# Kernel optimization log

Measured on AMD Instinct MI355X. Metric: run time of the kernel, lower is better.

Reference implementation:

```python
import jax, jax.numpy as jnp
import numpy as np

# --- static configuration (mirrors init_kwargs) ---
L = 16        # latent_size
HL = 512      # hypernet_layer_size
D = 64        # decoder_layer_size
NDEC = 2      # decoder_n_layers
B, G = 128, 100  # batch, grid (pressure levels)
LOGP_MEAN, LOGP_STD = 0.0, 3.0
T_MEAN, T_STD = 1500.0, 500.0

# decoder layer structure generated by the hypernet
WEIGHT_SIZES = [(1, D)] + [(D, D)] * NDEC + [(D, 1)]
BIAS_SIZES = [1] + [D] * NDEC + [1]
OUT_SIZE = sum(a * b for a, b in WEIGHT_SIZES) + sum(BIAS_SIZES)  # 8450


def setup_inputs() -> dict:
    key = jax.random.key(0)
    ks = jax.random.split(key, 8)
    def init(k, shape, fan_in):
        return (jax.random.normal(k, shape, jnp.float32) / np.float32(np.sqrt(fan_in)))
    return {
        "z": jax.random.normal(ks[0], (B, L), jnp.float32),
        "log_P": jax.random.normal(ks[1], (B, G), jnp.float32) * 2.0,
        # hypernet MLP params: L -> HL -> HL -> HL -> OUT_SIZE
        "hW0": init(ks[2], (L, HL), L), "hb0": jnp.zeros((HL,), jnp.float32),
        "hW1": init(ks[3], (HL, HL), HL), "hb1": jnp.zeros((HL,), jnp.float32),
        "hW2": init(ks[4], (HL, HL), HL), "hb2": jnp.zeros((HL,), jnp.float32),
        "hWo": init(ks[5], (HL, OUT_SIZE), HL), "hbo": jnp.zeros((OUT_SIZE,), jnp.float32),
    }


def reference(z, log_P, hW0, hb0, hW1, hb1, hW2, hb2, hWo, hbo):
    Bsz, Gsz = log_P.shape
    R = Bsz * Gsz  # flattened rows
    # broadcast latent over the pressure grid: (B, L) -> (R, L)
    z_flat = jnp.broadcast_to(z[:, None, :], (Bsz, Gsz, z.shape[-1])).reshape(R, -1)
    # normalize pressure -> decoder input, shape (R, 1)
    x = (log_P.reshape(R, 1) - LOGP_MEAN) / LOGP_STD
    # hypernet MLP (leaky_relu, slope 0.01 like torch default)
    h = jax.nn.leaky_relu(z_flat @ hW0 + hb0)
    h = jax.nn.leaky_relu(h @ hW1 + hb1)
    h = jax.nn.leaky_relu(h @ hW2 + hb2)
    wab = h @ hWo + hbo  # (R, OUT_SIZE): per-row decoder weights+biases
    # per-row decoder: chain of batched GEMVs with siren activation
    off = 0
    n_layers = len(WEIGHT_SIZES)
    for i, ((di, do), bs) in enumerate(zip(WEIGHT_SIZES, BIAS_SIZES)):
        n = di * do
        w = wab[:, off:off + n].reshape(R, di, do)
        b = wab[:, off + n:off + n + bs]  # broadcasts against (R, do)
        off += n + bs
        x = jnp.einsum('bi,bij->bj', x, w) + b
        if i == 0:
            x = x * 30.0  # siren first-layer omega_0
        if i < n_layers - 1:
            x = jnp.sin(x)  # siren activation; last layer is Identity
    T_pred = x.reshape(Bsz, Gsz)
    # undo temperature normalization
    return T_pred * T_STD + T_MEAN
```

## Files before the change

kernel.cpp:

```cpp
#include <hip/hip_runtime.h>

#define WSTRIDE 8704
#define DSTR 68

__device__ __forceinline__ float lrelu(float x) { return x > 0.0f ? x : 0.01f * x; }

__global__ __launch_bounds__(128) void h0T_kernel(const float* __restrict__ z,
                                                  const float* __restrict__ W,
                                                  const float* __restrict__ bias,
                                                  float* __restrict__ h0T) {
    int j = blockIdx.x;
    int b = threadIdx.x;
    float zr[16];
    *(float4*)&zr[0]  = *(const float4*)&z[b * 16 + 0];
    *(float4*)&zr[4]  = *(const float4*)&z[b * 16 + 4];
    *(float4*)&zr[8]  = *(const float4*)&z[b * 16 + 8];
    *(float4*)&zr[12] = *(const float4*)&z[b * 16 + 12];
    float acc = bias[j];
#pragma unroll
    for (int l = 0; l < 16; ++l) acc = fmaf(zr[l], W[l * 512 + j], acc);
    h0T[j * 128 + b] = lrelu(acc);
}

__global__ __launch_bounds__(512) void gemmT_kernel(const float* __restrict__ At,
                                                    const float* __restrict__ W,
                                                    const float* __restrict__ bias,
                                                    float* __restrict__ OT) {
    __shared__ float red[8][64][13];
    int jt = blockIdx.x & 7;
    int bt = blockIdx.x >> 3;
    int lane = threadIdx.x & 63;
    int wid  = __builtin_amdgcn_readfirstlane(threadIdx.x >> 6);
    int j = jt * 64 + lane;
    int b0 = bt * 8;
    float acc[8] = {};
    int k0 = wid * 64;
#pragma unroll 4
    for (int kk = 0; kk < 64; ++kk) {
        int k = k0 + kk;
        const float* __restrict__ a = At + k * 128 + b0;
        float w = W[k * 512 + j];
#pragma unroll
        for (int i = 0; i < 8; ++i) acc[i] = fmaf(a[i], w, acc[i]);
    }
#pragma unroll
    for (int i = 0; i < 8; ++i) red[wid][lane][i] = acc[i];
    __syncthreads();
    int jj = threadIdx.x >> 3;
    int bb = threadIdx.x & 7;
    float s = 0.f;
#pragma unroll
    for (int w = 0; w < 8; ++w) s += red[w][jj][bb];
    int jg = jt * 64 + jj;
    OT[jg * 128 + b0 + bb] = lrelu(s + bias[jg]);
}

__global__ __launch_bounds__(256) void wabT_kernel(const float* __restrict__ At,
                                                   const float* __restrict__ W,
                                                   const float* __restrict__ bias,
                                                   float* __restrict__ wab) {
    __shared__ float red[4][128][13];
    int tid = threadIdx.x;
    if (blockIdx.x == 1152) {
        int b = tid & 127;
        int jc = 8448 + (tid >> 7);
        float acc = 0.f;
#pragma unroll 8
        for (int k = 0; k < 512; ++k)
            acc = fmaf(At[k * 128 + b], W[k * 8450 + jc], acc);
        wab[b * WSTRIDE + jc] = acc + bias[jc];
        return;
    }
    int xcd = blockIdx.x & 7;
    int idx = blockIdx.x >> 3;
    int jt = (idx >> 4) * 8 + xcd;
    int bt = idx & 15;
    if (jt >= 66) return;
    int lane = tid & 63;
    int wid  = __builtin_amdgcn_readfirstlane(tid >> 6);
    int j = jt * 128 + lane * 2;
    int b0 = bt * 8;
    float acc[8][2] = {};
    int k0 = wid * 128;
#pragma unroll 4
    for (int kk = 0; kk < 128; ++kk) {
        int k = k0 + kk;
        const float* __restrict__ a = At + k * 128 + b0;
        float2 w = *(const float2*)&W[k * 8450 + j];
#pragma unroll
        for (int i = 0; i < 8; ++i) {
            acc[i][0] = fmaf(a[i], w.x, acc[i][0]);
            acc[i][1] = fmaf(a[i], w.y, acc[i][1]);
        }
    }
#pragma unroll
    for (int i = 0; i < 8; ++i) {
        red[wid][lane * 2 + 0][i] = acc[i][0];
        red[wid][lane * 2 + 1][i] = acc[i][1];
    }
    __syncthreads();
    int jj = tid & 127;
    int half = tid >> 7;
    int jg = jt * 128 + jj;
    float bj = bias[jg];
#pragma unroll
    for (int q = 0; q < 4; ++q) {
        int bb = half * 4 + q;
        float s = red[0][jj][bb] + red[1][jj][bb] + red[2][jj][bb] + red[3][jj][bb];
        wab[(b0 + bb) * WSTRIDE + jg] = s + bj;
    }
}

__global__ __launch_bounds__(256) void decoder_kernel(const float* __restrict__ wab,
                                                      const float* __restrict__ logP,
                                                      float* __restrict__ out) {
    __shared__ __align__(16) float hA[64 * DSTR];
    __shared__ __align__(16) float hB[64 * DSTR];
    __shared__ float red[4][68];
    int b   = blockIdx.x >> 1;
    int gbl = blockIdx.x & 1;
    int lane = threadIdx.x & 63;
    int wid  = __builtin_amdgcn_readfirstlane(threadIdx.x >> 6);
    int jq = wid * 16;
    int g = gbl * 64 + lane;
    bool act = g < 100;
    const float* __restrict__ row = wab + b * WSTRIDE;
    float x0 = act ? logP[b * 100 + g] * (1.0f / 3.0f) : 0.0f;

    float c0 = row[64];
#pragma unroll
    for (int t4 = 0; t4 < 4; ++t4) {
        float4 v;
        v.x = __sinf(30.0f * fmaf(x0, row[jq + t4*4 + 0], c0));
        v.y = __sinf(30.0f * fmaf(x0, row[jq + t4*4 + 1], c0));
        v.z = __sinf(30.0f * fmaf(x0, row[jq + t4*4 + 2], c0));
        v.w = __sinf(30.0f * fmaf(x0, row[jq + t4*4 + 3], c0));
        *(float4*)&hA[lane * DSTR + jq + t4 * 4] = v;
    }
    __syncthreads();

    {
        float a[16];
#pragma unroll
        for (int t = 0; t < 16; ++t) a[t] = row[4161 + jq + t];
#pragma unroll 4
        for (int i4 = 0; i4 < 16; ++i4) {
            float4 hv = *(const float4*)&hA[lane * DSTR + i4 * 4];
#pragma unroll
            for (int e = 0; e < 4; ++e) {
                int i = i4 * 4 + e;
                const float* __restrict__ wr = row + 65 + i * 64 + jq;
                float hi = (&hv.x)[e];
#pragma unroll
                for (int t = 0; t < 16; ++t) a[t] = fmaf(hi, wr[t], a[t]);
            }
        }
#pragma unroll
        for (int t4 = 0; t4 < 4; ++t4) {
            float4 v;
            v.x = __sinf(a[t4*4 + 0]); v.y = __sinf(a[t4*4 + 1]);
            v.z = __sinf(a[t4*4 + 2]); v.w = __sinf(a[t4*4 + 3]);
            *(float4*)&hB[lane * DSTR + jq + t4 * 4] = v;
        }
    }
    __syncthreads();

    {
        float a[16];
#pragma unroll
        for (int t = 0; t < 16; ++t) a[t] = row[8321 + jq + t];
#pragma unroll 4
        for (int i4 = 0; i4 < 16; ++i4) {
            float4 hv = *(const float4*)&hB[lane * DSTR + i4 * 4];
#pragma unroll
            for (int e = 0; e < 4; ++e) {
                int i = i4 * 4 + e;
                const float* __restrict__ wr = row + 4225 + i * 64 + jq;
                float hi = (&hv.x)[e];
#pragma unroll
                for (int t = 0; t < 16; ++t) a[t] = fmaf(hi, wr[t], a[t]);
            }
        }
#pragma unroll
        for (int t4 = 0; t4 < 4; ++t4) {
            float4 v;
            v.x = __sinf(a[t4*4 + 0]); v.y = __sinf(a[t4*4 + 1]);
            v.z = __sinf(a[t4*4 + 2]); v.w = __sinf(a[t4*4 + 3]);
            *(float4*)&hA[lane * DSTR + jq + t4 * 4] = v;
        }
    }
    __syncthreads();

    float p = 0.f;
#pragma unroll
    for (int t4 = 0; t4 < 4; ++t4) {
        float4 hv = *(const float4*)&hA[lane * DSTR + jq + t4 * 4];
        p = fmaf(hv.x, row[8385 + jq + t4*4 + 0], p);
        p = fmaf(hv.y, row[8385 + jq + t4*4 + 1], p);
        p = fmaf(hv.z, row[8385 + jq + t4*4 + 2], p);
        p = fmaf(hv.w, row[8385 + jq + t4*4 + 3], p);
    }
    red[wid][lane] = p;
    __syncthreads();
    if (wid == 0 && act) {
        float s = red[0][lane] + red[1][lane] + red[2][lane] + red[3][lane] + row[8449];
        out[b * 100 + g] = fmaf(s, 500.0f, 1500.0f);
    }
}

extern "C" void kernel_launch(void* const* d_in, const int* in_sizes, int n_in,
                              void* d_out, int out_size, void* d_ws, size_t ws_size,
                              hipStream_t stream) {
    const float* z    = (const float*)d_in[0];
    const float* logP = (const float*)d_in[1];
    const float* hW0  = (const float*)d_in[2];
    const float* hb0  = (const float*)d_in[3];
    const float* hW1  = (const float*)d_in[4];
    const float* hb1  = (const float*)d_in[5];
    const float* hW2  = (const float*)d_in[6];
    const float* hb2  = (const float*)d_in[7];
    const float* hWo  = (const float*)d_in[8];
    const float* hbo  = (const float*)d_in[9];
    float* out = (float*)d_out;

    float* wab = (float*)d_ws;
    float* h0T = wab + 128 * WSTRIDE;
    float* h1T = h0T + 512 * 128;
    float* h2T = h1T + 512 * 128;

    h0T_kernel<<<512, 128, 0, stream>>>(z, hW0, hb0, h0T);
    gemmT_kernel<<<128, 512, 0, stream>>>(h0T, hW1, hb1, h1T);
    gemmT_kernel<<<128, 512, 0, stream>>>(h1T, hW2, hb2, h2T);
    wabT_kernel<<<1153, 256, 0, stream>>>(h2T, hWo, hbo, wab);
    decoder_kernel<<<256, 256, 0, stream>>>(wab, logP, out);
}
```

Before: 74.99 us.

## Stage activations and decoder weights in LDS, retile hypernet GEMMs

The hidden-layer GEMMs now stage the activation tile in shared memory and use 4 batch rows per block with 256 threads, doubling the grid. The output GEMM stages a 16-row activation tile in LDS, uses 16x2 register tiles per thread, and halves the block count with a new XCD-aware mapping. The decoder copies each 64x64 weight matrix into LDS once and reads it with vectorized broadcast loads instead of repeated global loads, and stores hidden states transposed with a padded stride. This adds LDS traffic and extra syncs, and the output GEMM has less parallelism.

```diff
diff --git a/kernel.cpp b/kernel.cpp
--- a/kernel.cpp
+++ b/kernel.cpp
@@ -1,7 +1,7 @@
 #include <hip/hip_runtime.h>
 
 #define WSTRIDE 8704
-#define DSTR 68
+#define GSTR 65
 
 __device__ __forceinline__ float lrelu(float x) { return x > 0.0f ? x : 0.01f * x; }
 
@@ -22,35 +22,44 @@
     h0T[j * 128 + b] = lrelu(acc);
 }
 
-__global__ __launch_bounds__(512) void gemmT_kernel(const float* __restrict__ At,
+__global__ __launch_bounds__(256) void gemmT_kernel(const float* __restrict__ At,
                                                     const float* __restrict__ W,
                                                     const float* __restrict__ bias,
                                                     float* __restrict__ OT) {
-    __shared__ float red[8][64][13];
+    __shared__ __align__(16) float As[512][4];
+    __shared__ float red[4][64][5];
     int jt = blockIdx.x & 7;
     int bt = blockIdx.x >> 3;
-    int lane = threadIdx.x & 63;
-    int wid  = __builtin_amdgcn_readfirstlane(threadIdx.x >> 6);
+    int tid = threadIdx.x;
+    int lane = tid & 63;
+    int wid  = __builtin_amdgcn_readfirstlane(tid >> 6);
+    int b0 = bt * 4;
+#pragma unroll
+    for (int r = 0; r < 4; ++r) {
+        int p = r * 256 + tid;
+        int k = p >> 1, q = p & 1;
+        *(float2*)&As[k][q * 2] = *(const float2*)&At[k * 128 + b0 + q * 2];
+    }
+    __syncthreads();
     int j = jt * 64 + lane;
-    int b0 = bt * 8;
-    float acc[8] = {};
-    int k0 = wid * 64;
-#pragma unroll 4
-    for (int kk = 0; kk < 64; ++kk) {
+    float acc[4] = {};
+    int k0 = wid * 128;
+#pragma unroll 8
+    for (int kk = 0; kk < 128; ++kk) {
         int k = k0 + kk;
-        const float* __restrict__ a = At + k * 128 + b0;
+        float4 a = *(const float4*)&As[k][0];
         float w = W[k * 512 + j];
-#pragma unroll
-        for (int i = 0; i < 8; ++i) acc[i] = fmaf(a[i], w, acc[i]);
-    }
-#pragma unroll
-    for (int i = 0; i < 8; ++i) red[wid][lane][i] = acc[i];
-    __syncthreads();
-    int jj = threadIdx.x >> 3;
-    int bb = threadIdx.x & 7;
-    float s = 0.f;
-#pragma unroll
-    for (int w = 0; w < 8; ++w) s += red[w][jj][bb];
+        acc[0] = fmaf(a.x, w, acc[0]);
+        acc[1] = fmaf(a.y, w, acc[1]);
+        acc[2] = fmaf(a.z, w, acc[2]);
+        acc[3] = fmaf(a.w, w, acc[3]);
+    }
+#pragma unroll
+    for (int i = 0; i < 4; ++i) red[wid][lane][i] = acc[i];
+    __syncthreads();
+    int jj = tid >> 2;
+    int bb = tid & 3;
+    float s = red[0][jj][bb] + red[1][jj][bb] + red[2][jj][bb] + red[3][jj][bb];
     int jg = jt * 64 + jj;
     OT[jg * 128 + b0 + bb] = lrelu(s + bias[jg]);
 }
@@ -59,54 +68,73 @@
                                                    const float* __restrict__ W,
                                                    const float* __restrict__ bias,
                                                    float* __restrict__ wab) {
-    __shared__ float red[4][128][13];
+    __shared__ __align__(16) float As[512][16];
+    __shared__ float red[4][64][33];
     int tid = threadIdx.x;
-    if (blockIdx.x == 1152) {
+    if (blockIdx.x == 528) {
         int b = tid & 127;
         int jc = 8448 + (tid >> 7);
-        float acc = 0.f;
-#pragma unroll 8
-        for (int k = 0; k < 512; ++k)
-            acc = fmaf(At[k * 128 + b], W[k * 8450 + jc], acc);
-        wab[b * WSTRIDE + jc] = acc + bias[jc];
+        float a0 = 0.f, a1 = 0.f, a2 = 0.f, a3 = 0.f;
+#pragma unroll 4
+        for (int k4 = 0; k4 < 128; ++k4) {
+            a0 = fmaf(At[(k4*4+0) * 128 + b], W[(k4*4+0) * 8450 + jc], a0);
+            a1 = fmaf(At[(k4*4+1) * 128 + b], W[(k4*4+1) * 8450 + jc], a1);
+            a2 = fmaf(At[(k4*4+2) * 128 + b], W[(k4*4+2) * 8450 + jc], a2);
+            a3 = fmaf(At[(k4*4+3) * 128 + b], W[(k4*4+3) * 8450 + jc], a3);
+        }
+        wab[b * WSTRIDE + jc] = a0 + a1 + a2 + a3 + bias[jc];
         return;
     }
-    int xcd = blockIdx.x & 7;
-    int idx = blockIdx.x >> 3;
-    int jt = (idx >> 4) * 8 + xcd;
-    int bt = idx & 15;
-    if (jt >= 66) return;
+    int v = (blockIdx.x & 7) * 66 + (blockIdx.x >> 3);
+    int jt = v >> 3;
+    int bt = v & 7;
     int lane = tid & 63;
     int wid  = __builtin_amdgcn_readfirstlane(tid >> 6);
-    int j = jt * 128 + lane * 2;
-    int b0 = bt * 8;
-    float acc[8][2] = {};
+    int b0 = bt * 16;
+#pragma unroll
+    for (int r = 0; r < 16; ++r) {
+        int p = r * 256 + tid;
+        int k = p >> 3, q = p & 7;
+        *(float2*)&As[k][q * 2] = *(const float2*)&At[k * 128 + b0 + q * 2];
+    }
+    __syncthreads();
+    int j0 = jt * 128 + lane * 2;
+    float acc[16][2] = {};
     int k0 = wid * 128;
 #pragma unroll 4
     for (int kk = 0; kk < 128; ++kk) {
         int k = k0 + kk;
-        const float* __restrict__ a = At + k * 128 + b0;
-        float2 w = *(const float2*)&W[k * 8450 + j];
-#pragma unroll
-        for (int i = 0; i < 8; ++i) {
-            acc[i][0] = fmaf(a[i], w.x, acc[i][0]);
-            acc[i][1] = fmaf(a[i], w.y, acc[i][1]);
-        }
-    }
-#pragma unroll
-    for (int i = 0; i < 8; ++i) {
-        red[wid][lane * 2 + 0][i] = acc[i][0];
-        red[wid][lane * 2 + 1][i] = acc[i][1];
-    }
-    __syncthreads();
-    int jj = tid & 127;
-    int half = tid >> 7;
+        float4 a0 = *(const float4*)&As[k][0];
+        float4 a1 = *(const float4*)&As[k][4];
+        float4 a2 = *(const float4*)&As[k][8];
+        float4 a3 = *(const float4*)&As[k][12];
+        float2 w = *(const float2*)&W[k * 8450 + j0];
+        float av[16] = {a0.x,a0.y,a0.z,a0.w, a1.x,a1.y,a1.z,a1.w,
+                        a2.x,a2.y,a2.z,a2.w, a3.x,a3.y,a3.z,a3.w};
+#pragma unroll
+        for (int bb = 0; bb < 16; ++bb) {
+            acc[bb][0] = fmaf(av[bb], w.x, acc[bb][0]);
+            acc[bb][1] = fmaf(av[bb], w.y, acc[bb][1]);
+        }
+    }
+#pragma unroll
+    for (int bb = 0; bb < 16; ++bb) {
+        red[wid][lane][bb * 2 + 0] = acc[bb][0];
+        red[wid][lane][bb * 2 + 1] = acc[bb][1];
+    }
+    __syncthreads();
+    int jj = tid >> 1;
+    int bh = tid & 1;
+    int lane_r = jj >> 1;
+    int jl = jj & 1;
     int jg = jt * 128 + jj;
     float bj = bias[jg];
 #pragma unroll
-    for (int q = 0; q < 4; ++q) {
-        int bb = half * 4 + q;
-        float s = red[0][jj][bb] + red[1][jj][bb] + red[2][jj][bb] + red[3][jj][bb];
+    for (int bq = 0; bq < 8; ++bq) {
+        int bb = bh * 8 + bq;
+        int idx = bb * 2 + jl;
+        float s = red[0][lane_r][idx] + red[1][lane_r][idx]
+                + red[2][lane_r][idx] + red[3][lane_r][idx];
         wab[(b0 + bb) * WSTRIDE + jg] = s + bj;
     }
 }
@@ -114,13 +142,15 @@
 __global__ __launch_bounds__(256) void decoder_kernel(const float* __restrict__ wab,
                                                       const float* __restrict__ logP,
                                                       float* __restrict__ out) {
-    __shared__ __align__(16) float hA[64 * DSTR];
-    __shared__ __align__(16) float hB[64 * DSTR];
+    __shared__ __align__(16) float Wl[64 * 64];
+    __shared__ float hX[64 * GSTR];
+    __shared__ float hY[64 * GSTR];
     __shared__ float red[4][68];
     int b   = blockIdx.x >> 1;
     int gbl = blockIdx.x & 1;
-    int lane = threadIdx.x & 63;
-    int wid  = __builtin_amdgcn_readfirstlane(threadIdx.x >> 6);
+    int tid = threadIdx.x;
+    int lane = tid & 63;
+    int wid  = __builtin_amdgcn_readfirstlane(tid >> 6);
     int jq = wid * 16;
     int g = gbl * 64 + lane;
     bool act = g < 100;
@@ -129,13 +159,12 @@
 
     float c0 = row[64];
 #pragma unroll
-    for (int t4 = 0; t4 < 4; ++t4) {
-        float4 v;
-        v.x = __sinf(30.0f * fmaf(x0, row[jq + t4*4 + 0], c0));
-        v.y = __sinf(30.0f * fmaf(x0, row[jq + t4*4 + 1], c0));
-        v.z = __sinf(30.0f * fmaf(x0, row[jq + t4*4 + 2], c0));
-        v.w = __sinf(30.0f * fmaf(x0, row[jq + t4*4 + 3], c0));
-        *(float4*)&hA[lane * DSTR + jq + t4 * 4] = v;
+    for (int t = 0; t < 16; ++t)
+        hX[(jq + t) * GSTR + lane] = __sinf(30.0f * fmaf(x0, row[jq + t], c0));
+#pragma unroll
+    for (int r = 0; r < 16; ++r) {
+        int idx = r * 256 + tid;
+        Wl[idx] = row[65 + idx];
     }
     __syncthreads();
 
@@ -144,24 +173,30 @@
 #pragma unroll
         for (int t = 0; t < 16; ++t) a[t] = row[4161 + jq + t];
 #pragma unroll 4
-        for (int i4 = 0; i4 < 16; ++i4) {
-            float4 hv = *(const float4*)&hA[lane * DSTR + i4 * 4];
-#pragma unroll
-            for (int e = 0; e < 4; ++e) {
-                int i = i4 * 4 + e;
-                const float* __restrict__ wr = row + 65 + i * 64 + jq;
-                float hi = (&hv.x)[e];
-#pragma unroll
-                for (int t = 0; t < 16; ++t) a[t] = fmaf(hi, wr[t], a[t]);
-            }
-        }
-#pragma unroll
-        for (int t4 = 0; t4 < 4; ++t4) {
-            float4 v;
-            v.x = __sinf(a[t4*4 + 0]); v.y = __sinf(a[t4*4 + 1]);
-            v.z = __sinf(a[t4*4 + 2]); v.w = __sinf(a[t4*4 + 3]);
-            *(float4*)&hB[lane * DSTR + jq + t4 * 4] = v;
-        }
+        for (int i = 0; i < 64; ++i) {
+            float hi = hX[i * GSTR + lane];
+            const float* wr = &Wl[i * 64 + jq];
+            float4 w0 = *(const float4*)&wr[0];
+            float4 w1 = *(const float4*)&wr[4];
+            float4 w2 = *(const float4*)&wr[8];
+            float4 w3 = *(const float4*)&wr[12];
+            a[0]  = fmaf(hi, w0.x, a[0]);  a[1]  = fmaf(hi, w0.y, a[1]);
+            a[2]  = fmaf(hi, w0.z, a[2]);  a[3]  = fmaf(hi, w0.w, a[3]);
+            a[4]  = fmaf(hi, w1.x, a[4]);  a[5]  = fmaf(hi, w1.y, a[5]);
+            a[6]  = fmaf(hi, w1.z, a[6]);  a[7]  = fmaf(hi, w1.w, a[7]);
+            a[8]  = fmaf(hi, w2.x, a[8]);  a[9]  = fmaf(hi, w2.y, a[9]);
+            a[10] = fmaf(hi, w2.z, a[10]); a[11] = fmaf(hi, w2.w, a[11]);
+            a[12] = fmaf(hi, w3.x, a[12]); a[13] = fmaf(hi, w3.y, a[13]);
+            a[14] = fmaf(hi, w3.z, a[14]); a[15] = fmaf(hi, w3.w, a[15]);
+        }
+#pragma unroll
+        for (int t = 0; t < 16; ++t) hY[(jq + t) * GSTR + lane] = __sinf(a[t]);
+    }
+    __syncthreads();
+#pragma unroll
+    for (int r = 0; r < 16; ++r) {
+        int idx = r * 256 + tid;
+        Wl[idx] = row[4225 + idx];
     }
     __syncthreads();
 
@@ -170,36 +205,31 @@
 #pragma unroll
         for (int t = 0; t < 16; ++t) a[t] = row[8321 + jq + t];
 #pragma unroll 4
-        for (int i4 = 0; i4 < 16; ++i4) {
-            float4 hv = *(const float4*)&hB[lane * DSTR + i4 * 4];
-#pragma unroll
-            for (int e = 0; e < 4; ++e) {
-                int i = i4 * 4 + e;
-                const float* __restrict__ wr = row + 4225 + i * 64 + jq;
-                float hi = (&hv.x)[e];
-#pragma unroll
-                for (int t = 0; t < 16; ++t) a[t] = fmaf(hi, wr[t], a[t]);
-            }
-        }
-#pragma unroll
-        for (int t4 = 0; t4 < 4; ++t4) {
-            float4 v;
-            v.x = __sinf(a[t4*4 + 0]); v.y = __sinf(a[t4*4 + 1]);
-            v.z = __sinf(a[t4*4 + 2]); v.w = __sinf(a[t4*4 + 3]);
-            *(float4*)&hA[lane * DSTR + jq + t4 * 4] = v;
-        }
+        for (int i = 0; i < 64; ++i) {
+            float hi = hY[i * GSTR + lane];
+            const float* wr = &Wl[i * 64 + jq];
+            float4 w0 = *(const float4*)&wr[0];
+            float4 w1 = *(const float4*)&wr[4];
+            float4 w2 = *(const float4*)&wr[8];
+            float4 w3 = *(const float4*)&wr[12];
+            a[0]  = fmaf(hi, w0.x, a[0]);  a[1]  = fmaf(hi, w0.y, a[1]);
+            a[2]  = fmaf(hi, w0.z, a[2]);  a[3]  = fmaf(hi, w0.w, a[3]);
+            a[4]  = fmaf(hi, w1.x, a[4]);  a[5]  = fmaf(hi, w1.y, a[5]);
+            a[6]  = fmaf(hi, w1.z, a[6]);  a[7]  = fmaf(hi, w1.w, a[7]);
+            a[8]  = fmaf(hi, w2.x, a[8]);  a[9]  = fmaf(hi, w2.y, a[9]);
+            a[10] = fmaf(hi, w2.z, a[10]); a[11] = fmaf(hi, w2.w, a[11]);
+            a[12] = fmaf(hi, w3.x, a[12]); a[13] = fmaf(hi, w3.y, a[13]);
+            a[14] = fmaf(hi, w3.z, a[14]); a[15] = fmaf(hi, w3.w, a[15]);
+        }
+#pragma unroll
+        for (int t = 0; t < 16; ++t) hX[(jq + t) * GSTR + lane] = __sinf(a[t]);
     }
     __syncthreads();
 
     float p = 0.f;
 #pragma unroll
-    for (int t4 = 0; t4 < 4; ++t4) {
-        float4 hv = *(const float4*)&hA[lane * DSTR + jq + t4 * 4];
-        p = fmaf(hv.x, row[8385 + jq + t4*4 + 0], p);
-        p = fmaf(hv.y, row[8385 + jq + t4*4 + 1], p);
-        p = fmaf(hv.z, row[8385 + jq + t4*4 + 2], p);
-        p = fmaf(hv.w, row[8385 + jq + t4*4 + 3], p);
-    }
+    for (int t = 0; t < 16; ++t)
+        p = fmaf(hX[(jq + t) * GSTR + lane], row[8385 + jq + t], p);
     red[wid][lane] = p;
     __syncthreads();
     if (wid == 0 && act) {
@@ -229,8 +259,8 @@
     float* h2T = h1T + 512 * 128;
 
     h0T_kernel<<<512, 128, 0, stream>>>(z, hW0, hb0, h0T);
-    gemmT_kernel<<<128, 512, 0, stream>>>(h0T, hW1, hb1, h1T);
-    gemmT_kernel<<<128, 512, 0, stream>>>(h1T, hW2, hb2, h2T);
-    wabT_kernel<<<1153, 256, 0, stream>>>(h2T, hWo, hbo, wab);
+    gemmT_kernel<<<256, 256, 0, stream>>>(h0T, hW1, hb1, h1T);
+    gemmT_kernel<<<256, 256, 0, stream>>>(h1T, hW2, hb2, h2T);
+    wabT_kernel<<<529, 256, 0, stream>>>(h2T, hWo, hbo, wab);
     decoder_kernel<<<256, 256, 0, stream>>>(wab, logP, out);
 }
```

Result: faster. 72.71 us (-3.0%).
